# Optimization experiments

Measured on AMD Instinct MI355X. Metric: run time of the kernel, lower is better.

Reference implementation:

```python
import math
import jax, jax.numpy as jnp
import numpy as np

D_MODEL = 1024
N_HEADS = 16
D_K = D_MODEL // N_HEADS


def setup_inputs() -> dict:
    key = jax.random.key(0)
    ks = jax.random.split(key, 12)
    B, L, D = 8, 2048, D_MODEL
    scale = 1.0 / math.sqrt(D)
    inp = {
        "queries": jax.random.normal(ks[0], (B, L, D), jnp.float32),
        "keys": jax.random.normal(ks[1], (B, L, D), jnp.float32),
        "values": jax.random.normal(ks[2], (B, L, D), jnp.float32),
        "Wq": jax.random.normal(ks[3], (D, D), jnp.float32) * scale,
        "bq": jnp.zeros((D,), jnp.float32),
        "Wk": jax.random.normal(ks[4], (D, D), jnp.float32) * scale,
        "bk": jnp.zeros((D,), jnp.float32),
        "Wv": jax.random.normal(ks[5], (D, D), jnp.float32) * scale,
        "bv": jnp.zeros((D,), jnp.float32),
        "Wo": jax.random.normal(ks[6], (D, D), jnp.float32) * scale,
        "bo": jnp.zeros((D,), jnp.float32),
    }
    return inp


def _autocorr_forward(queries, keys, values, Wq, bq, Wk, bk, Wv, bv, Wo, bo):
    B, L, D = queries.shape
    H, dk = N_HEADS, D_K
    # projections (torch Linear: x @ W.T + b), split heads -> [B, L, H, dk]
    q = (queries @ Wq.T + bq).reshape(B, L, H, dk)
    k = (keys @ Wk.T + bk).reshape(B, L, H, dk)
    v = (values @ Wv.T + bv).reshape(B, L, H, dk)

    # FFT cross-correlation along time, averaged over channel dim: [B, L, H]
    qf = jnp.fft.rfft(q, axis=1)
    kf = jnp.fft.rfft(k, axis=1)
    corr = jnp.fft.irfft(qf * jnp.conj(kf), n=L, axis=1).mean(axis=-1)
    corr = corr.transpose(0, 2, 1)  # [B, H, L]

    topk = min(max(1, int(math.log(L))), L)  # top_k=None default
    weights, delays = jax.lax.top_k(corr, topk)  # [B, H, k]
    w = jax.nn.softmax(weights, axis=-1)

    # modulo-shifted gather indices: [B, H, k, L]
    idx = (jnp.arange(L)[None, None, None, :] - delays[..., None]) % L
    v_h = v.transpose(0, 2, 1, 3)  # [B, H, L, dk]
    # gather shifted copies: [B, H, k, L, dk]
    gathered = jnp.take_along_axis(v_h[:, :, None], idx[..., None], axis=3)
    out = (w[..., None, None] * gathered).sum(axis=2)  # [B, H, L, dk]

    out = out.transpose(0, 2, 1, 3).reshape(B, L, D)
    return out @ Wo.T + bo


def reference(queries, keys, values, Wq, bq, Wk, bk, Wv, bv, Wo, bo):
    return _autocorr_forward(queries, keys, values, Wq, bq, Wk, bk, Wv, bv, Wo, bo)
```

## Files before the change

kernel.cpp:

```cpp
#include <hip/hip_runtime.h>
#include <hip/hip_bf16.h>
#include <math.h>

#define B_SZ 8
#define L_SZ 2048
#define D_SZ 1024
#define H_SZ 16
#define DK_SZ 64
#define TOPK 7
#define M_SZ (B_SZ * L_SZ)

typedef __attribute__((ext_vector_type(8))) short short8;
typedef __attribute__((ext_vector_type(4))) float float4v;
typedef unsigned short ushort_t;
typedef unsigned int uint_t;

__device__ __forceinline__ ushort_t f2bf(float x) {
    uint_t u = __float_as_uint(x);
    uint_t r = (u + 0x7fffu + ((u >> 16) & 1u)) >> 16;
    return (ushort_t)r;
}

__device__ __forceinline__ void split8(float4 x, float4 y, short8& hi, short8& lo) {
    float f[8] = {x.x, x.y, x.z, x.w, y.x, y.y, y.z, y.w};
#pragma unroll
    for (int i = 0; i < 8; ++i) {
        uint_t b = __float_as_uint(f[i]);
        hi[i] = (short)(b >> 16);
        float r = f[i] - __uint_as_float(b & 0xffff0000u);
        lo[i] = (short)(__float_as_uint(r) >> 16);
    }
}

__device__ __forceinline__ void gl_lds16(const ushort_t* g, ushort_t* l) {
    __builtin_amdgcn_global_load_lds(
        (const __attribute__((address_space(1))) unsigned int*)g,
        (__attribute__((address_space(3))) unsigned int*)l, 16, 0, 0);
}

__global__ __launch_bounds__(256)
void zero_f32(float* __restrict__ p, int n4) {
    int i = blockIdx.x * 256 + threadIdx.x;
    if (i < n4) ((float4*)p)[i] = make_float4(0.f, 0.f, 0.f, 0.f);
}

__global__ __launch_bounds__(256)
void split_fp32(const float* __restrict__ X, ushort_t* __restrict__ hi,
                ushort_t* __restrict__ lo, int n8) {
    int i = blockIdx.x * 256 + threadIdx.x;
    if (i >= n8) return;
    float4 a = ((const float4*)X)[2 * i];
    float4 b = ((const float4*)X)[2 * i + 1];
    short8 h, l;
    split8(a, b, h, l);
    *(short8*)(hi + (size_t)i * 8) = h;
    *(short8*)(lo + (size_t)i * 8) = l;
}

template <bool BF16OUT>
__global__ __launch_bounds__(256)
void gemm_split_mfma(const float* __restrict__ X, const ushort_t* __restrict__ Whi,
                     const ushort_t* __restrict__ Wlo, const float* __restrict__ bias,
                     void* __restrict__ Yv, int M, int N, int K) {
    __shared__ __align__(16) short Ah[4][128][8];
    __shared__ __align__(16) short Al[4][128][8];
    __shared__ __align__(16) short Bh[4][128][8];
    __shared__ __align__(16) short Bl[4][128][8];

    const int tid = threadIdx.x;
    const int lane = tid & 63;
    const int wave = tid >> 6;
    const int wm = wave >> 1, wn = wave & 1;

    const int flat = blockIdx.y * gridDim.x + blockIdx.x;
    const int cpx  = (gridDim.x * gridDim.y) >> 3;
    const int swz  = (flat & 7) * cpx + (flat >> 3);
    const int bx   = swz % gridDim.x;
    const int by   = swz / gridDim.x;
    const size_t m0 = (size_t)by * 128;
    const size_t n0 = (size_t)bx * 128;

    const int srow = tid >> 1;
    const int g0 = (tid & 1) * 2;
    const int skseg = (tid & 1) * 16;

    const float*    Xp  = X   + (m0 + srow) * K + skseg;
    const ushort_t* Whp = Whi + (n0 + srow) * K + skseg;
    const ushort_t* Wlp = Wlo + (n0 + srow) * K + skseg;

    const int fr = lane & 15;
    const int fg = lane >> 4;

    float4 ax0 = *(const float4*)(Xp + 0);
    float4 ax1 = *(const float4*)(Xp + 4);
    float4 ax2 = *(const float4*)(Xp + 8);
    float4 ax3 = *(const float4*)(Xp + 12);
    short8 bh0 = *(const short8*)(Whp + 0);
    short8 bh1 = *(const short8*)(Whp + 8);
    short8 bl0 = *(const short8*)(Wlp + 0);
    short8 bl1 = *(const short8*)(Wlp + 8);

    float4v acc[4][4];
#pragma unroll
    for (int i = 0; i < 4; ++i)
#pragma unroll
        for (int j = 0; j < 4; ++j) acc[i][j] = (float4v){0.f, 0.f, 0.f, 0.f};

    for (int k0 = 0; k0 < K; k0 += 32) {
        __syncthreads();
        short8 h, l;
        split8(ax0, ax1, h, l);
        *(short8*)&Ah[g0][srow][0] = h;      *(short8*)&Al[g0][srow][0] = l;
        split8(ax2, ax3, h, l);
        *(short8*)&Ah[g0 + 1][srow][0] = h;  *(short8*)&Al[g0 + 1][srow][0] = l;
        *(short8*)&Bh[g0][srow][0] = bh0;    *(short8*)&Bh[g0 + 1][srow][0] = bh1;
        *(short8*)&Bl[g0][srow][0] = bl0;    *(short8*)&Bl[g0 + 1][srow][0] = bl1;
        __syncthreads();

        if (k0 + 32 < K) {
            ax0 = *(const float4*)(Xp + k0 + 32);
            ax1 = *(const float4*)(Xp + k0 + 36);
            ax2 = *(const float4*)(Xp + k0 + 40);
            ax3 = *(const float4*)(Xp + k0 + 44);
            bh0 = *(const short8*)(Whp + k0 + 32);
            bh1 = *(const short8*)(Whp + k0 + 40);
            bl0 = *(const short8*)(Wlp + k0 + 32);
            bl1 = *(const short8*)(Wlp + k0 + 40);
        }

        short8 afh[4], afl[4], bfh[4], bfl[4];
#pragma unroll
        for (int i = 0; i < 4; ++i) {
            const int r = wm * 64 + i * 16 + fr;
            afh[i] = *(const short8*)&Ah[fg][r][0];
            afl[i] = *(const short8*)&Al[fg][r][0];
        }
#pragma unroll
        for (int j = 0; j < 4; ++j) {
            const int r = wn * 64 + j * 16 + fr;
            bfh[j] = *(const short8*)&Bh[fg][r][0];
            bfl[j] = *(const short8*)&Bl[fg][r][0];
        }
#pragma unroll
        for (int i = 0; i < 4; ++i)
#pragma unroll
            for (int j = 0; j < 4; ++j) {
                acc[i][j] = __builtin_amdgcn_mfma_f32_16x16x32_bf16(afh[i], bfh[j], acc[i][j], 0, 0, 0);
                acc[i][j] = __builtin_amdgcn_mfma_f32_16x16x32_bf16(afh[i], bfl[j], acc[i][j], 0, 0, 0);
                acc[i][j] = __builtin_amdgcn_mfma_f32_16x16x32_bf16(afl[i], bfh[j], acc[i][j], 0, 0, 0);
            }
    }

    const int en = fr;
    const int emb = (lane >> 4) * 4;
#pragma unroll
    for (int j = 0; j < 4; ++j) {
        const size_t col = n0 + wn * 64 + j * 16 + en;
        const float bv = bias[col];
#pragma unroll
        for (int i = 0; i < 4; ++i) {
#pragma unroll
            for (int r = 0; r < 4; ++r) {
                const size_t row = m0 + wm * 64 + i * 16 + emb + r;
                const float o = acc[i][j][r] + bv;
                if (BF16OUT) ((ushort_t*)Yv)[row * N + col] = f2bf(o);
                else         ((float*)Yv)[row * N + col] = o;
            }
        }
    }
}

__global__ __launch_bounds__(256)
void corr_mfma(const ushort_t* __restrict__ Qb, const ushort_t* __restrict__ Kb,
               float* __restrict__ corr) {
    __shared__ __align__(16) ushort_t Qlds[28 * 1024];
    __shared__ __align__(16) ushort_t Klds[4 * 1024];

    const int tid  = threadIdx.x;
    const int wave = tid >> 6;
    const int lane = tid & 63;
    const int bh = blockIdx.x;
    const int jq = blockIdx.y;
    const int b = bh >> 4, h = bh & 15;
    const int b0 = jq * 32;
    const int jbase = b0 + wave * 8;
    const int rr = lane & 15;
    const int cq = lane >> 4;
    const int s7 = rr & 7;

    const size_t slice = (size_t)b * L_SZ * D_SZ + (size_t)h * DK_SZ;
    const ushort_t* Qs = Qb + slice;
    const ushort_t* Ks = Kb + slice;
    const ushort_t* Qp = Qs + cq * 8;

    const int st  = tid & 127;
    const int sr  = st >> 3;
    const int sc  = (st & 7) ^ (sr & 7);
    const int whalf = (wave & 1) * 512;

    const int roff0 = rr * 64 + ((cq ^ s7) * 8);
    const int roff1 = roff0 ^ 32;

    float4v acc[8];
#pragma unroll
    for (int i = 0; i < 8; ++i) acc[i] = (float4v){0.f, 0.f, 0.f, 0.f};

    if (wave < 2) {
        for (int i = 0; i < 26; ++i) {
            const int qt = (b0 + 8 + i) & 127;
            gl_lds16(Qs + (size_t)(qt * 16 + sr) * 1024 + sc * 8,
                     &Qlds[i * 1024 + whalf]);
        }
    } else {
        for (int i = 0; i < 3; ++i) {
            gl_lds16(Ks + (size_t)(i * 16 + sr) * 1024 + sc * 8,
                     &Klds[i * 1024 + whalf]);
        }
    }

    short8 Wa[8], Wb[8];
#pragma unroll
    for (int i = 0; i < 8; ++i) {
        const size_t tq = (size_t)((((jbase + i) & 127) << 4) + rr) * D_SZ;
        Wa[i] = *(const short8*)(Qp + tq);
        Wb[i] = *(const short8*)(Qp + tq + 32);
    }

    asm volatile("s_waitcnt vmcnt(0)" ::: "memory");
    __builtin_amdgcn_s_barrier();
    asm volatile("" ::: "memory");

    short8 kb0 = *(const short8*)&Klds[roff0];
    short8 kb1 = *(const short8*)&Klds[roff1];

    int qsr = wave * 8;
    int qsw = 26;

    for (int s8 = 0; s8 < 128; s8 += 8) {
#pragma unroll
        for (int u = 0; u < 8; ++u) {
            const int s0 = s8 + u;
            if (wave < 2) {
                const int qt = (b0 + 34 + s0) & 127;
                gl_lds16(Qs + (size_t)(qt * 16 + sr) * 1024 + sc * 8,
                         &Qlds[qsw * 1024 + whalf]);
            } else {
                const int kt = (s0 + 3) & 127;
                gl_lds16(Ks + (size_t)(kt * 16 + sr) * 1024 + sc * 8,
                         &Klds[((s0 + 3) & 3) * 1024 + whalf]);
            }
            asm volatile("s_waitcnt vmcnt(2)" ::: "memory");
            __builtin_amdgcn_s_barrier();
            asm volatile("" ::: "memory");

            const int kslot = ((s0 + 1) & 3) * 1024;
            short8 nk0 = *(const short8*)&Klds[kslot + roff0];
            short8 nk1 = *(const short8*)&Klds[kslot + roff1];

            acc[0] = __builtin_amdgcn_mfma_f32_16x16x32_bf16(Wa[u], kb0, acc[0], 0, 0, 0);
            acc[0] = __builtin_amdgcn_mfma_f32_16x16x32_bf16(Wb[u], kb1, acc[0], 0, 0, 0);
            {
                const int qbse = qsr * 1024;
                Wa[u] = *(const short8*)&Qlds[qbse + roff0];
                Wb[u] = *(const short8*)&Qlds[qbse + roff1];
            }
#pragma unroll
            for (int jj = 1; jj < 8; ++jj) {
                acc[jj] = __builtin_amdgcn_mfma_f32_16x16x32_bf16(Wa[(u + jj) & 7], kb0, acc[jj], 0, 0, 0);
                acc[jj] = __builtin_amdgcn_mfma_f32_16x16x32_bf16(Wb[(u + jj) & 7], kb1, acc[jj], 0, 0, 0);
            }
            kb0 = nk0; kb1 = nk1;
            qsr = (qsr + 1 == 28) ? 0 : qsr + 1;
            qsw = (qsw + 1 == 28) ? 0 : qsw + 1;
        }
    }

    const int n = lane & 15;
    const int mb = (lane >> 4) * 4;
    float* cb = corr + (size_t)bh * L_SZ;
#pragma unroll
    for (int jj = 0; jj < 8; ++jj) {
        const int j16 = (jbase + jj) << 4;
#pragma unroll
        for (int r = 0; r < 4; ++r) {
            const int d = (j16 + mb + r - n) & (L_SZ - 1);
            atomicAdd(cb + d, acc[jj][r] * (1.0f / 64.0f));
        }
    }
}

__global__ __launch_bounds__(256)
void topk_softmax(const float* __restrict__ corr, float* __restrict__ w,
                  int* __restrict__ delays) {
    __shared__ float cv[L_SZ];
    __shared__ float rv[256];
    __shared__ int   ri[256];
    __shared__ float topv[TOPK];
    __shared__ int   topi[TOPK];
    const int bh = blockIdx.x, tid = threadIdx.x;

    for (int i = tid; i < L_SZ; i += 256) cv[i] = corr[(size_t)bh * L_SZ + i];
    __syncthreads();

    for (int it = 0; it < TOPK; ++it) {
        float best = -INFINITY; int bi = 0;
        for (int i = tid; i < L_SZ; i += 256) {
            float x = cv[i];
            if (x > best) { best = x; bi = i; }
        }
        rv[tid] = best; ri[tid] = bi;
        __syncthreads();
        for (int stride = 128; stride > 0; stride >>= 1) {
            if (tid < stride) {
                float ov = rv[tid + stride]; int oi = ri[tid + stride];
                if (ov > rv[tid] || (ov == rv[tid] && oi < ri[tid])) {
                    rv[tid] = ov; ri[tid] = oi;
                }
            }
            __syncthreads();
        }
        if (tid == 0) {
            topv[it] = rv[0]; topi[it] = ri[0];
            cv[ri[0]] = -INFINITY;
        }
        __syncthreads();
    }

    if (tid == 0) {
        float mx = topv[0];
        float e[TOPK], s = 0.f;
#pragma unroll
        for (int i = 0; i < TOPK; ++i) { e[i] = expf(topv[i] - mx); s += e[i]; }
        const float inv = 1.0f / s;
#pragma unroll
        for (int i = 0; i < TOPK; ++i) {
            w[bh * TOPK + i] = e[i] * inv;
            delays[bh * TOPK + i] = topi[i];
        }
    }
}

__global__ __launch_bounds__(256)
void gather_combine(const float* __restrict__ V, const float* __restrict__ w,
                    const int* __restrict__ delays, float* __restrict__ mid) {
    const size_t g = (size_t)blockIdx.x * 256 + threadIdx.x;
    const int c4 = (int)(g & 255);
    const int t  = (int)((g >> 8) & (L_SZ - 1));
    const int b  = (int)(g >> 19);
    const int h  = c4 >> 4;
    const int bh = b * H_SZ + h;
    const size_t colbase = (size_t)b * L_SZ * D_SZ + (size_t)c4 * 4;

    float4 acc = {0.f, 0.f, 0.f, 0.f};
#pragma unroll
    for (int i = 0; i < TOPK; ++i) {
        const float wi = w[bh * TOPK + i];
        const int   di = delays[bh * TOPK + i];
        const int   ts = (t - di) & (L_SZ - 1);
        float4 v4 = *(const float4*)(V + colbase + (size_t)ts * D_SZ);
        acc.x += wi * v4.x; acc.y += wi * v4.y;
        acc.z += wi * v4.z; acc.w += wi * v4.w;
    }
    *(float4*)(mid + (size_t)b * L_SZ * D_SZ + (size_t)t * D_SZ + c4 * 4) = acc;
}

extern "C" void kernel_launch(void* const* d_in, const int* in_sizes, int n_in,
                              void* d_out, int out_size, void* d_ws, size_t ws_size,
                              hipStream_t stream) {
    const float* queries = (const float*)d_in[0];
    const float* keys    = (const float*)d_in[1];
    const float* values  = (const float*)d_in[2];
    const float* Wq = (const float*)d_in[3];
    const float* bq = (const float*)d_in[4];
    const float* Wk = (const float*)d_in[5];
    const float* bk = (const float*)d_in[6];
    const float* Wv = (const float*)d_in[7];
    const float* bv = (const float*)d_in[8];
    const float* Wo = (const float*)d_in[9];
    const float* bo = (const float*)d_in[10];

    const size_t NE = (size_t)M_SZ * D_SZ;
    ushort_t* Qb16 = (ushort_t*)d_ws;
    ushort_t* Kb16 = Qb16 + NE;
    float* Vb   = (float*)(Kb16 + NE);
    float* corr = Vb + NE;
    float* wbuf = corr + (size_t)B_SZ * H_SZ * L_SZ;
    int*   dbuf = (int*)(wbuf + B_SZ * H_SZ * TOPK);
    ushort_t* WH = (ushort_t*)(dbuf + B_SZ * H_SZ * TOPK);
    ushort_t* WL = WH + (size_t)D_SZ * D_SZ;
    float* mid  = (float*)d_ws;

    dim3 ggemm(D_SZ / 128, M_SZ / 128);
    const int wn8 = D_SZ * D_SZ / 8;

    split_fp32<<<(wn8 + 255) / 256, 256, 0, stream>>>(Wq, WH, WL, wn8);
    gemm_split_mfma<true><<<ggemm, 256, 0, stream>>>(queries, WH, WL, bq, Qb16, M_SZ, D_SZ, D_SZ);
    split_fp32<<<(wn8 + 255) / 256, 256, 0, stream>>>(Wk, WH, WL, wn8);
    gemm_split_mfma<true><<<ggemm, 256, 0, stream>>>(keys, WH, WL, bk, Kb16, M_SZ, D_SZ, D_SZ);
    split_fp32<<<(wn8 + 255) / 256, 256, 0, stream>>>(Wv, WH, WL, wn8);
    gemm_split_mfma<false><<<ggemm, 256, 0, stream>>>(values, WH, WL, bv, Vb, M_SZ, D_SZ, D_SZ);

    zero_f32<<<(B_SZ * H_SZ * L_SZ / 4 + 255) / 256, 256, 0, stream>>>(
        corr, B_SZ * H_SZ * L_SZ / 4);

    corr_mfma<<<dim3(B_SZ * H_SZ, 4), 256, 0, stream>>>(Qb16, Kb16, corr);

    topk_softmax<<<B_SZ * H_SZ, 256, 0, stream>>>(corr, wbuf, dbuf);

    gather_combine<<<(M_SZ * 256) / 256, 256, 0, stream>>>(Vb, wbuf, dbuf, mid);

    split_fp32<<<(wn8 + 255) / 256, 256, 0, stream>>>(Wo, WH, WL, wn8);
    gemm_split_mfma<false><<<ggemm, 256, 0, stream>>>(mid, WH, WL, bo, (float*)d_out, M_SZ, D_SZ, D_SZ);
}
```

Baseline: 795.8 us.

## Pipeline split-bf16 GEMM with async global-to-LDS loads and swizzled LDS buffers

Restructures the projection GEMM main loop into a multi-stage pipeline. Weight tiles are fetched with direct global-to-LDS loads into a triple buffer two steps ahead, and activations are split and written into a double-buffered LDS tile, so there is one barrier per K step instead of two. LDS layouts use an XOR swizzle to avoid bank conflicts, and MFMA sections raise wave priority. The cost is more LDS use and hand-written waitcnt bookkeeping that must stay correct.

```diff
diff --git a/kernel.cpp b/kernel.cpp
--- a/kernel.cpp
+++ b/kernel.cpp
@@ -62,10 +62,8 @@
 void gemm_split_mfma(const float* __restrict__ X, const ushort_t* __restrict__ Whi,
                      const ushort_t* __restrict__ Wlo, const float* __restrict__ bias,
                      void* __restrict__ Yv, int M, int N, int K) {
-    __shared__ __align__(16) short Ah[4][128][8];
-    __shared__ __align__(16) short Al[4][128][8];
-    __shared__ __align__(16) short Bh[4][128][8];
-    __shared__ __align__(16) short Bl[4][128][8];
+    __shared__ __align__(16) ushort_t Alds[2][2][128][4][8];
+    __shared__ __align__(16) ushort_t Blds[3][2][128][4][8];
 
     const int tid = threadIdx.x;
     const int lane = tid & 63;
@@ -74,73 +72,104 @@
 
     const int flat = blockIdx.y * gridDim.x + blockIdx.x;
     const int cpx  = (gridDim.x * gridDim.y) >> 3;
-    const int swz  = (flat & 7) * cpx + (flat >> 3);
-    const int bx   = swz % gridDim.x;
-    const int by   = swz / gridDim.x;
+    const int swzb = (flat & 7) * cpx + (flat >> 3);
+    const int bx   = swzb % gridDim.x;
+    const int by   = swzb / gridDim.x;
     const size_t m0 = (size_t)by * 128;
     const size_t n0 = (size_t)bx * 128;
 
-    const int srow = tid >> 1;
-    const int g0 = (tid & 1) * 2;
-    const int skseg = (tid & 1) * 16;
-
-    const float*    Xp  = X   + (m0 + srow) * K + skseg;
-    const ushort_t* Whp = Whi + (n0 + srow) * K + skseg;
-    const ushort_t* Wlp = Wlo + (n0 + srow) * K + skseg;
+    const int NT = K >> 5;
+
+    const int arow = tid >> 1;
+    const int g0   = (tid & 1) * 2;
+    const int sA   = (arow ^ (arow >> 2)) & 3;
+    const int c00  = g0 ^ sA, c01 = (g0 + 1) ^ sA;
+    const float* Xp = X + (m0 + arow) * K + (tid & 1) * 16;
+    ushort_t* Awr = &Alds[0][0][arow][0][0];
+
+    const ushort_t* bptr[4];
+    int blbase[4];
+#pragma unroll
+    for (int i = 0; i < 4; ++i) {
+        const int GB  = wave * 256 + i * 64 + lane;
+        const int arr = GB >> 9;
+        const int row = (GB >> 2) & 127;
+        const int c   = GB & 3;
+        const int gs  = c ^ ((row ^ (row >> 2)) & 3);
+        bptr[i]   = (arr ? Wlo : Whi) + (n0 + row) * K + gs * 8;
+        blbase[i] = wave * 2048 + i * 512;
+    }
 
     const int fr = lane & 15;
     const int fg = lane >> 4;
+    int offA[4], offB[4];
+#pragma unroll
+    for (int i = 0; i < 4; ++i) {
+        const int ra = wm * 64 + i * 16 + fr;
+        offA[i] = ra * 32 + (fg ^ ((ra ^ (ra >> 2)) & 3)) * 8;
+        const int rb = wn * 64 + i * 16 + fr;
+        offB[i] = rb * 32 + (fg ^ ((rb ^ (rb >> 2)) & 3)) * 8;
+    }
+
+    float4v acc[4][4];
+#pragma unroll
+    for (int i = 0; i < 4; ++i)
+#pragma unroll
+        for (int j = 0; j < 4; ++j) acc[i][j] = (float4v){0.f, 0.f, 0.f, 0.f};
 
     float4 ax0 = *(const float4*)(Xp + 0);
     float4 ax1 = *(const float4*)(Xp + 4);
     float4 ax2 = *(const float4*)(Xp + 8);
     float4 ax3 = *(const float4*)(Xp + 12);
-    short8 bh0 = *(const short8*)(Whp + 0);
-    short8 bh1 = *(const short8*)(Whp + 8);
-    short8 bl0 = *(const short8*)(Wlp + 0);
-    short8 bl1 = *(const short8*)(Wlp + 8);
-
-    float4v acc[4][4];
-#pragma unroll
-    for (int i = 0; i < 4; ++i)
-#pragma unroll
-        for (int j = 0; j < 4; ++j) acc[i][j] = (float4v){0.f, 0.f, 0.f, 0.f};
-
-    for (int k0 = 0; k0 < K; k0 += 32) {
-        __syncthreads();
+#pragma unroll
+    for (int i = 0; i < 4; ++i) gl_lds16(bptr[i],      &Blds[0][0][0][0][0] + blbase[i]);
+#pragma unroll
+    for (int i = 0; i < 4; ++i) gl_lds16(bptr[i] + 32, &Blds[1][0][0][0][0] + blbase[i]);
+    {
         short8 h, l;
         split8(ax0, ax1, h, l);
-        *(short8*)&Ah[g0][srow][0] = h;      *(short8*)&Al[g0][srow][0] = l;
+        *(short8*)(Awr + c00 * 8) = h;  *(short8*)(Awr + 4096 + c00 * 8) = l;
         split8(ax2, ax3, h, l);
-        *(short8*)&Ah[g0 + 1][srow][0] = h;  *(short8*)&Al[g0 + 1][srow][0] = l;
-        *(short8*)&Bh[g0][srow][0] = bh0;    *(short8*)&Bh[g0 + 1][srow][0] = bh1;
-        *(short8*)&Bl[g0][srow][0] = bl0;    *(short8*)&Bl[g0 + 1][srow][0] = bl1;
-        __syncthreads();
-
-        if (k0 + 32 < K) {
-            ax0 = *(const float4*)(Xp + k0 + 32);
-            ax1 = *(const float4*)(Xp + k0 + 36);
-            ax2 = *(const float4*)(Xp + k0 + 40);
-            ax3 = *(const float4*)(Xp + k0 + 44);
-            bh0 = *(const short8*)(Whp + k0 + 32);
-            bh1 = *(const short8*)(Whp + k0 + 40);
-            bl0 = *(const short8*)(Wlp + k0 + 32);
-            bl1 = *(const short8*)(Wlp + k0 + 40);
-        }
-
+        *(short8*)(Awr + c01 * 8) = h;  *(short8*)(Awr + 4096 + c01 * 8) = l;
+    }
+    asm volatile("s_waitcnt lgkmcnt(0)" ::: "memory");
+    asm volatile("s_waitcnt vmcnt(4)" ::: "memory");
+    __builtin_amdgcn_s_barrier();
+    asm volatile("" ::: "memory");
+
+    int sa = 0;
+    int sb = 0;
+    for (int t = 0; t < NT; ++t) {
+        const int tn1 = (t + 1) & (NT - 1);
+        const int tn2 = (t + 2) & (NT - 1);
+        const int san = sa ^ 1;
+        const int sbn2 = (sb + 2 >= 3) ? sb - 1 : sb + 2;
+
+        const int ka = tn1 * 32;
+        ax0 = *(const float4*)(Xp + ka + 0);
+        ax1 = *(const float4*)(Xp + ka + 4);
+        ax2 = *(const float4*)(Xp + ka + 8);
+        ax3 = *(const float4*)(Xp + ka + 12);
+
+        {
+            const int kt = tn2 * 32;
+            ushort_t* sbase = &Blds[sbn2][0][0][0][0];
+#pragma unroll
+            for (int i = 0; i < 4; ++i) gl_lds16(bptr[i] + kt, sbase + blbase[i]);
+        }
+
+        const ushort_t* Ab = &Alds[sa][0][0][0][0];
+        const ushort_t* Bb = &Blds[sb][0][0][0][0];
         short8 afh[4], afl[4], bfh[4], bfl[4];
 #pragma unroll
         for (int i = 0; i < 4; ++i) {
-            const int r = wm * 64 + i * 16 + fr;
-            afh[i] = *(const short8*)&Ah[fg][r][0];
-            afl[i] = *(const short8*)&Al[fg][r][0];
-        }
-#pragma unroll
-        for (int j = 0; j < 4; ++j) {
-            const int r = wn * 64 + j * 16 + fr;
-            bfh[j] = *(const short8*)&Bh[fg][r][0];
-            bfl[j] = *(const short8*)&Bl[fg][r][0];
-        }
+            afh[i] = *(const short8*)(Ab + offA[i]);
+            afl[i] = *(const short8*)(Ab + 4096 + offA[i]);
+            bfh[i] = *(const short8*)(Bb + offB[i]);
+            bfl[i] = *(const short8*)(Bb + 4096 + offB[i]);
+        }
+
+        __builtin_amdgcn_s_setprio(1);
 #pragma unroll
         for (int i = 0; i < 4; ++i)
 #pragma unroll
@@ -149,7 +178,26 @@
                 acc[i][j] = __builtin_amdgcn_mfma_f32_16x16x32_bf16(afh[i], bfl[j], acc[i][j], 0, 0, 0);
                 acc[i][j] = __builtin_amdgcn_mfma_f32_16x16x32_bf16(afl[i], bfh[j], acc[i][j], 0, 0, 0);
             }
-    }
+        __builtin_amdgcn_s_setprio(0);
+
+        {
+            ushort_t* Aw = Awr + san * 8192;
+            short8 h, l;
+            split8(ax0, ax1, h, l);
+            *(short8*)(Aw + c00 * 8) = h;  *(short8*)(Aw + 4096 + c00 * 8) = l;
+            split8(ax2, ax3, h, l);
+            *(short8*)(Aw + c01 * 8) = h;  *(short8*)(Aw + 4096 + c01 * 8) = l;
+        }
+
+        asm volatile("s_waitcnt lgkmcnt(0)" ::: "memory");
+        asm volatile("s_waitcnt vmcnt(4)" ::: "memory");
+        __builtin_amdgcn_s_barrier();
+        asm volatile("" ::: "memory");
+
+        sa = san;
+        sb = (sb + 1 == 3) ? 0 : sb + 1;
+    }
+    asm volatile("s_waitcnt vmcnt(0)" ::: "memory");
 
     const int en = fr;
     const int emb = (lane >> 4) * 4;
```

New measurement: 878.3 us. +10.4%, slower.
